# Kernel tuning notes

Measured on AMD Instinct MI355X. Metric: run time of the kernel, lower is better.

## Reference

```python
import jax, jax.numpy as jnp
import numpy as np

N_ITER = 3  # affine-invariant Karcher mean iterations (mean_options['n_iterations'])
EPS = 1e-12


def _sym(A):
    return 0.5 * (A + jnp.swapaxes(A, -1, -2))


def _eig_fun(A, fn):
    # Apply spectral function fn to symmetric matrix/matrices A: V diag(fn(w)) V^T
    w, V = jnp.linalg.eigh(A)
    return jnp.einsum('...ij,...j,...kj->...ik', V, fn(w), V)


def _logm(A):
    return _eig_fun(A, lambda w: jnp.log(jnp.maximum(w, EPS)))


def _expm(A):
    return _eig_fun(A, jnp.exp)


def _sqrtm(A):
    return _eig_fun(A, lambda w: jnp.sqrt(jnp.maximum(w, 0.0)))


def _invsqrtm(A):
    return _eig_fun(A, lambda w: 1.0 / jnp.sqrt(jnp.maximum(w, EPS)))


def _affine_invariant_mean(data, n_iterations):
    # Karcher mean: init at arithmetic mean, fixed-point iterations on the manifold
    M = jnp.mean(data, axis=0)
    for _ in range(n_iterations):
        Ms = _sqrtm(M)
        Mi = _invsqrtm(M)
        T = jnp.mean(_logm(Mi @ data @ Mi), axis=0)  # (n, n) tangent mean
        M = Ms @ _expm(T) @ Ms
    return _sym(M)


def setup_inputs() -> dict:
    key = jax.random.key(0)
    k1, k2 = jax.random.split(key)
    B, n = 8192, 64
    X = jax.random.normal(k1, (B, n, n), dtype=jnp.float32)
    # SPD batch: X X^T / n + 0.1 I
    data = jnp.einsum('bij,bkj->bik', X, X) / n + 0.1 * jnp.eye(n, dtype=jnp.float32)
    bias_param = 0.1 * jax.random.normal(k2, (n, n), dtype=jnp.float32)
    return {"data": data, "bias_param": bias_param}


def reference(data, bias_param):
    # 1) batch mean on the SPD manifold (affine-invariant Karcher mean)
    mean = _affine_invariant_mean(data, N_ITER)
    # 2) whitening: G data G with G = mean^{-1/2}
    G = _invsqrtm(mean)
    data_normalized = G @ data @ G
    # 3) bias congruence: Covbias = expm(sym(bias_param)) (log-Euclidean param),
    #    S = Covbias^{1/2} = expm(sym(bias_param)/2); out = S X S
    S = _eig_fun(_sym(bias_param), lambda w: jnp.exp(0.5 * w))
    return S @ data_normalized @ S
```

## Files before the change

### kernel.cpp

```cpp
#include <hip/hip_runtime.h>
#include <cmath>

#ifndef M_PI
#define M_PI 3.14159265358979323846
#endif

#define K_CHEB 48
#define A_CHEB 0.05
#define B_CHEB 14.0
#define PS_S 7
#define PS_Q 6

typedef __attribute__((ext_vector_type(8))) short bhalf8;
typedef __attribute__((ext_vector_type(16))) float f32x16;

struct PSArg {
  float mid, invhalf;
  float a[PS_Q + 1][PS_S];
};


__device__ __forceinline__ unsigned cvt_pk_bf16(float a, float b) {
  unsigned r;
  asm("v_cvt_pk_bf16_f32 %0, %1, %2" : "=v"(r) : "v"(a), "v"(b));
  return r;
}

__device__ __forceinline__ void split4_store(short* __restrict__ Xh, short* __restrict__ Xl,
                                             int off, float v0, float v1, float v2, float v3) {
  unsigned h01 = cvt_pk_bf16(v0, v1);
  unsigned h23 = cvt_pk_bf16(v2, v3);
  float r0 = v0 - __uint_as_float(h01 << 16);
  float r1 = v1 - __uint_as_float(h01 & 0xffff0000u);
  float r2 = v2 - __uint_as_float(h23 << 16);
  float r3 = v3 - __uint_as_float(h23 & 0xffff0000u);
  unsigned l01 = cvt_pk_bf16(r0, r1);
  unsigned l23 = cvt_pk_bf16(r2, r3);
  *(uint2*)(Xh + off) = make_uint2(h01, h23);
  *(uint2*)(Xl + off) = make_uint2(l01, l23);
}


__device__ __forceinline__ void stage64(const float* __restrict__ g, float* __restrict__ s, int tid) {
#pragma unroll
  for (int r = 0; r < 4; r++) {
    int idx = tid + 256 * r;
    *(float4*)(s + 4 * idx) = *(const float4*)(g + 4 * idx);
  }
}

__device__ __forceinline__ void store_tile(float* __restrict__ S, int r0, int c0, const float t[16]) {
#pragma unroll
  for (int i = 0; i < 4; i++)
    *(float4*)(S + (r0 + i) * 64 + c0) = *(const float4*)(&t[4 * i]);
}

__device__ __forceinline__ void gemm_tile_sym(const float* __restrict__ A, const float* __restrict__ B,
                                              int r0, int c0, float t[16]) {
#pragma unroll
  for (int i = 0; i < 16; i++) t[i] = 0.f;
#pragma unroll 4
  for (int k = 0; k < 64; k += 4) {
    float a[16], b[16];
#pragma unroll
    for (int kk = 0; kk < 4; kk++) {
      *(float4*)(&a[4 * kk]) = *(const float4*)(A + (k + kk) * 64 + r0);
      *(float4*)(&b[4 * kk]) = *(const float4*)(B + (k + kk) * 64 + c0);
    }
#pragma unroll
    for (int kk = 0; kk < 4; kk++)
#pragma unroll
      for (int i = 0; i < 4; i++)
#pragma unroll
        for (int j = 0; j < 4; j++)
          t[4 * i + j] += a[4 * kk + i] * b[4 * kk + j];
  }
}


__global__ __launch_bounds__(256) void reduce_mean8(const float* __restrict__ data,
                                                    float* __restrict__ part) {
  const size_t base = (size_t)blockIdx.x * 8 * 4096;
  const int tid = threadIdx.x;
#pragma unroll
  for (int r = 0; r < 4; r++) {
    int idx = tid + 256 * r;
    float4 s = make_float4(0.f, 0.f, 0.f, 0.f);
#pragma unroll
    for (int m = 0; m < 8; m++) {
      float4 v = *(const float4*)(data + base + (size_t)m * 4096 + 4 * idx);
      s.x += v.x; s.y += v.y; s.z += v.z; s.w += v.w;
    }
    *(float4*)(part + (size_t)blockIdx.x * 4096 + 4 * idx) = s;
  }
}

__global__ __launch_bounds__(256) void reduce_cols(const float* __restrict__ part,
                                                   float* __restrict__ outv,
                                                   int nparts, float scale) {
  __shared__ float s[3][64];
  const int jj = threadIdx.x & 63, gg = threadIdx.x >> 6;
  const int j = (blockIdx.x << 6) + jj;
  float sum = 0.f;
  for (int g = gg; g < nparts; g += 4)
    sum += part[(size_t)g * 4096 + j];
  if (gg) s[gg - 1][jj] = sum;
  __syncthreads();
  if (gg == 0) outv[j] = (sum + s[0][jj] + s[1][jj] + s[2][jj]) * scale;
}


#define LDX 72
#define MAT (64 * LDX)

__device__ __forceinline__ void load_afrags(const short* __restrict__ Xh, const short* __restrict__ Xl,
                                            int aoff, bhalf8 ah[4], bhalf8 al[4]) {
#pragma unroll
  for (int kb = 0; kb < 4; kb++) {
    ah[kb] = *(const bhalf8*)(Xh + aoff + 16 * kb);
    al[kb] = *(const bhalf8*)(Xl + aoff + 16 * kb);
  }
}

__device__ __forceinline__ f32x16 prod3(const bhalf8 ah[4], const bhalf8 al[4],
                                        const short* __restrict__ Bh, const short* __restrict__ Bl,
                                        int boff) {
  f32x16 acc;
#pragma unroll
  for (int t = 0; t < 16; t++) acc[t] = 0.f;
#pragma unroll
  for (int kb = 0; kb < 4; kb++) {
    bhalf8 bh = *(const bhalf8*)(Bh + boff + 16 * kb);
    bhalf8 bl = *(const bhalf8*)(Bl + boff + 16 * kb);
    acc = __builtin_amdgcn_mfma_f32_32x32x16_bf16(ah[kb], bh, acc, 0, 0, 0);
    acc = __builtin_amdgcn_mfma_f32_32x32x16_bf16(ah[kb], bl, acc, 0, 0, 0);
    acc = __builtin_amdgcn_mfma_f32_32x32x16_bf16(al[kb], bh, acc, 0, 0, 0);
  }
  return acc;
}

__device__ __forceinline__ void tstore16(short* __restrict__ Xh, short* __restrict__ Xl,
                                         int bcol, int R, int half, const f32x16 v) {
#pragma unroll
  for (int g = 0; g < 4; g++) {
    int off = bcol * LDX + 32 * R + 8 * g + 4 * half;
    split4_store(Xh, Xl, off, v[4 * g + 0], v[4 * g + 1], v[4 * g + 2], v[4 * g + 3]);
  }
}

__device__ __forceinline__ void stage_split(const float* __restrict__ g64,
                                            short* __restrict__ Xh, short* __restrict__ Xl,
                                            int tid) {
#pragma unroll
  for (int i = 0; i < 4; i++) {
    int idx = tid + 256 * i;
    float4 v = *(const float4*)(g64 + 4 * idx);
    int row = idx >> 4, col = (idx & 15) << 2;
    split4_store(Xh, Xl, row * LDX + col, v.x, v.y, v.z, v.w);
  }
}

__global__ __launch_bounds__(256, 2) void cheb_ps(const float* __restrict__ data,
                                                  const float* __restrict__ Mi,
                                                  float* __restrict__ partial,
                                                  PSArg co) {
  extern __shared__ __align__(16) short smem[];
  short* sMh  = smem;
  short* sMl  = sMh + MAT;
  short* sAh  = sMl + MAT;
  short* sAl  = sAh + MAT;
  short* sB0h = sAl + MAT;
  short* sB0l = sB0h + MAT;
  short* sB1h = sB0l + MAT;
  short* sB1l = sB1h + MAT;

  const int tid = threadIdx.x;
  const int lane = tid & 63, wv = tid >> 6;
  const int R = wv >> 1, C = wv & 1;
  const int ln31 = lane & 31, half = lane >> 5;
  const int aoff = (32 * R + ln31) * LDX + half * 8;
  const int bcol = 32 * C + ln31;
  const int boff = bcol * LDX + half * 8;
  const int dsel = bcol - 32 * R - 4 * half;

  stage_split(Mi, sMh, sMl, tid);

  f32x16 accTm;
#pragma unroll
  for (int t = 0; t < 16; t++) accTm[t] = 0.f;

  bhalf8 ah[4], al[4];
  __syncthreads();

#pragma unroll 1
  for (int m = 0; m < 8; m++) {
    stage_split(data + ((size_t)blockIdx.x * 8 + m) * 4096, sAh, sAl, tid);
    __syncthreads();

    load_afrags(sAh, sAl, aoff, ah, al);
    f32x16 acc = prod3(ah, al, sMh, sMl, boff);
    tstore16(sB0h, sB0l, bcol, R, half, acc);
    __syncthreads();

    load_afrags(sMh, sMl, aoff, ah, al);
    acc = prod3(ah, al, sB0h, sB0l, boff);
    f32x16 T1;
#pragma unroll
    for (int g = 0; g < 4; g++)
#pragma unroll
      for (int t = 0; t < 4; t++) {
        float a = acc[4 * g + t];
        if (8 * g + t == dsel) a -= co.mid;
        T1[4 * g + t] = a * co.invhalf;
      }
    tstore16(sAh, sAl, bcol, R, half, T1);
    __syncthreads();

    load_afrags(sAh, sAl, aoff, ah, al);

    f32x16 T2, T3, T4, T5, T6;
    acc = prod3(ah, al, sAh, sAl, boff);
#pragma unroll
    for (int g = 0; g < 4; g++)
#pragma unroll
      for (int t = 0; t < 4; t++)
        T2[4 * g + t] = 2.f * acc[4 * g + t] - ((8 * g + t == dsel) ? 1.f : 0.f);
    tstore16(sB0h, sB0l, bcol, R, half, T2);
    __syncthreads();

    acc = prod3(ah, al, sB0h, sB0l, boff);
#pragma unroll
    for (int t = 0; t < 16; t++) T3[t] = 2.f * acc[t] - T1[t];
    tstore16(sB1h, sB1l, bcol, R, half, T3);
    __syncthreads();

    acc = prod3(ah, al, sB1h, sB1l, boff);
#pragma unroll
    for (int t = 0; t < 16; t++) T4[t] = 2.f * acc[t] - T2[t];
    tstore16(sB0h, sB0l, bcol, R, half, T4);
    __syncthreads();

    acc = prod3(ah, al, sB0h, sB0l, boff);
#pragma unroll
    for (int t = 0; t < 16; t++) T5[t] = 2.f * acc[t] - T3[t];
    tstore16(sB1h, sB1l, bcol, R, half, T5);
    __syncthreads();

    acc = prod3(ah, al, sB1h, sB1l, boff);
#pragma unroll
    for (int t = 0; t < 16; t++) T6[t] = 2.f * acc[t] - T4[t];
    tstore16(sB1h == sB1h ? sB0h : sB0h, sB0l, bcol, R, half, T6);
    __syncthreads();

    acc = prod3(ah, al, sB0h, sB0l, boff);
    f32x16 Y7;
#pragma unroll
    for (int t = 0; t < 16; t++) Y7[t] = 2.f * acc[t] - T5[t];
    tstore16(sAh, sAl, bcol, R, half, Y7);
    __syncthreads();

    load_afrags(sAh, sAl, aoff, ah, al);
    f32x16 bq1, bq2;
#pragma unroll
    for (int g = 0; g < 4; g++)
#pragma unroll
      for (int t = 0; t < 4; t++) {
        int i = 4 * g + t;
        float v = co.a[6][1] * T1[i] + co.a[6][2] * T2[i] + co.a[6][3] * T3[i]
                + co.a[6][4] * T4[i] + co.a[6][5] * T5[i] + co.a[6][6] * T6[i];
        if (8 * g + t == dsel) v += co.a[6][0];
        bq1[i] = v; bq2[i] = 0.f;
      }
    tstore16(sB1h, sB1l, bcol, R, half, bq1);
    __syncthreads();

#pragma unroll
    for (int q = 5; q >= 1; q--) {
      const short* rh = (q & 1) ? sB1h : sB0h;
      const short* rl = (q & 1) ? sB1l : sB0l;
      short* wh = (q & 1) ? sB0h : sB1h;
      short* wl = (q & 1) ? sB0l : sB1l;
      acc = prod3(ah, al, rh, rl, boff);
      f32x16 nb;
#pragma unroll
      for (int g = 0; g < 4; g++)
#pragma unroll
        for (int t = 0; t < 4; t++) {
          int i = 4 * g + t;
          float gq = co.a[q][1] * T1[i] + co.a[q][2] * T2[i] + co.a[q][3] * T3[i]
                   + co.a[q][4] * T4[i] + co.a[q][5] * T5[i] + co.a[q][6] * T6[i];
          if (8 * g + t == dsel) gq += co.a[q][0];
          nb[i] = gq + 2.f * acc[i] - bq2[i];
        }
      bq2 = bq1; bq1 = nb;
      tstore16(wh, wl, bcol, R, half, bq1);
      __syncthreads();
    }

    acc = prod3(ah, al, sB0h, sB0l, boff);
#pragma unroll
    for (int g = 0; g < 4; g++)
#pragma unroll
      for (int t = 0; t < 4; t++) {
        int i = 4 * g + t;
        float g0 = co.a[0][1] * T1[i] + co.a[0][2] * T2[i] + co.a[0][3] * T3[i]
                 + co.a[0][4] * T4[i] + co.a[0][5] * T5[i] + co.a[0][6] * T6[i];
        if (8 * g + t == dsel) g0 += co.a[0][0];
        accTm[i] += g0 + acc[i] - bq2[i];
      }
  }

  float* pp = partial + (size_t)blockIdx.x * 4096;
#pragma unroll
  for (int g = 0; g < 4; g++)
#pragma unroll
    for (int t = 0; t < 4; t++)
      pp[(32 * R + 8 * g + 4 * half + t) * 64 + bcol] = accTm[4 * g + t];
}


__global__ __launch_bounds__(256) void invsqrt_series(const float* __restrict__ Min,
                                                      float* __restrict__ MiOut,
                                                      float* __restrict__ MsOut) {
  __shared__ float sM[4096], sE[4096], sE2[4096], sE3[4096];
  __shared__ float csh;
  const int tid = threadIdx.x;
  const int r0 = (tid >> 4) << 2, c0 = (tid & 15) << 2;

  stage64(Min, sM, tid);
  __syncthreads();
  if (tid == 0) {
    float s = 0.f;
    for (int i = 0; i < 64; i++) s += sM[i * 64 + i];
    csh = s * (1.f / 64.f);
  }
  __syncthreads();
  const float invc = 1.f / csh;
  for (int idx = tid; idx < 4096; idx += 256) {
    int r = idx >> 6, c = idx & 63;
    sE[idx] = 0.5f * (sM[idx] + sM[c * 64 + r]) * invc - ((r == c) ? 1.f : 0.f);
  }
  __syncthreads();

  float t[16];
  gemm_tile_sym(sE, sE, r0, c0, t);  store_tile(sE2, r0, c0, t); __syncthreads();
  gemm_tile_sym(sE2, sE, r0, c0, t); store_tile(sE3, r0, c0, t); __syncthreads();
  gemm_tile_sym(sE2, sE2, r0, c0, t); store_tile(sM, r0, c0, t); __syncthreads();
  float t5[16];
  gemm_tile_sym(sE2, sE3, r0, c0, t5);

  const float sc = sqrtf(csh), rsc = 1.f / sc;
#pragma unroll
  for (int i = 0; i < 4; i++)
#pragma unroll
    for (int j = 0; j < 4; j++) {
      int off = (r0 + i) * 64 + (c0 + j);
      float d = ((r0 + i) == (c0 + j)) ? 1.f : 0.f;
      float e = sE[off], e2 = sE2[off], e3 = sE3[off], e4 = sM[off], e5 = t5[4 * i + j];
      float mi = (d - 0.5f * e + 0.375f * e2 - 0.3125f * e3 + 0.2734375f * e4 - 0.24609375f * e5) * rsc;
      float ms = (d + 0.5f * e - 0.125f * e2 + 0.0625f * e3 - 0.0390625f * e4 + 0.02734375f * e5) * sc;
      MiOut[off] = mi;
      MsOut[off] = ms;
    }
}


__device__ void taylor_expm8(const float* __restrict__ sA, float* __restrict__ sR,
                             int tid, int r0, int c0, float postscale) {
  for (int idx = tid; idx < 4096; idx += 256) {
    int r = idx >> 6, c = idx & 63;
    sR[idx] = ((r == c) ? 1.f : 0.f) + sA[idx] * 0.125f;
  }
  __syncthreads();
  float t[16];
#pragma unroll 1
  for (int k = 7; k >= 1; k--) {
    gemm_tile_sym(sA, sR, r0, c0, t);
    __syncthreads();
    const float inv = 1.f / (float)k;
    const float fin = (k == 1) ? postscale : 1.f;
#pragma unroll
    for (int i = 0; i < 4; i++)
#pragma unroll
      for (int j = 0; j < 4; j++) {
        int off = (r0 + i) * 64 + (c0 + j);
        float d = ((r0 + i) == (c0 + j)) ? 1.f : 0.f;
        sR[off] = (d + t[4 * i + j] * inv) * fin;
      }
    __syncthreads();
  }
}

__global__ __launch_bounds__(256) void expm_update(const float* __restrict__ Tin,
                                                   const float* __restrict__ Msin,
                                                   float* __restrict__ Mout) {
  __shared__ float sA[4096], sR[4096], sB[4096];
  __shared__ float mush;
  const int tid = threadIdx.x;
  const int r0 = (tid >> 4) << 2, c0 = (tid & 15) << 2;

  stage64(Tin, sB, tid);
  __syncthreads();
  if (tid == 0) {
    float s = 0.f;
    for (int i = 0; i < 64; i++) s += sB[i * 64 + i];
    mush = s * (1.f / 64.f);
  }
  __syncthreads();
  const float mu = mush;
  for (int idx = tid; idx < 4096; idx += 256) {
    int r = idx >> 6, c = idx & 63;
    sA[idx] = 0.5f * (sB[idx] + sB[c * 64 + r]) - ((r == c) ? mu : 0.f);
  }
  __syncthreads();
  taylor_expm8(sA, sR, tid, r0, c0, expf(mu));

  stage64(Msin, sB, tid);
  __syncthreads();
  float t[16];
  gemm_tile_sym(sR, sB, r0, c0, t);
  store_tile(sA, r0, c0, t);
  __syncthreads();
  gemm_tile_sym(sB, sA, r0, c0, t);
#pragma unroll
  for (int i = 0; i < 4; i++)
    *(float4*)(Mout + (r0 + i) * 64 + c0) = *(const float4*)(&t[4 * i]);
}

__global__ __launch_bounds__(256) void bias_expm_P(const float* __restrict__ bias,
                                                   const float* __restrict__ Gin,
                                                   float* __restrict__ Pout) {
  __shared__ float sA[4096], sR[4096], sB[4096];
  const int tid = threadIdx.x;
  const int r0 = (tid >> 4) << 2, c0 = (tid & 15) << 2;

  stage64(bias, sB, tid);
  __syncthreads();
  for (int idx = tid; idx < 4096; idx += 256) {
    int r = idx >> 6, c = idx & 63;
    sA[idx] = 0.0625f * (sB[idx] + sB[c * 64 + r]);
  }
  __syncthreads();
  taylor_expm8(sA, sR, tid, r0, c0, 1.f);

  float t[16];
  gemm_tile_sym(sR, sR, r0, c0, t);
  store_tile(sB, r0, c0, t);
  __syncthreads();
  gemm_tile_sym(sB, sB, r0, c0, t);
  store_tile(sR, r0, c0, t);
  stage64(Gin, sA, tid);
  __syncthreads();
  gemm_tile_sym(sR, sA, r0, c0, t);
#pragma unroll
  for (int i = 0; i < 4; i++)
    *(float4*)(Pout + (r0 + i) * 64 + c0) = *(const float4*)(&t[4 * i]);
}

__global__ __launch_bounds__(256) void final_out(const float* __restrict__ data,
                                                 const float* __restrict__ Pin,
                                                 float* __restrict__ out) {
  __shared__ float sPT[4096], sD[4096], sT[4096];
  const int tid = threadIdx.x;
  const int r0 = (tid >> 4) << 2, c0 = (tid & 15) << 2;

  for (int idx = tid; idx < 4096; idx += 256) {
    int r = idx >> 6, c = idx & 63;
    sPT[c * 64 + r] = Pin[idx];
  }
  __syncthreads();
  float t[16];
#pragma unroll 1
  for (int m = 0; m < 8; m++) {
    size_t b = (size_t)blockIdx.x * 8 + m;
    stage64(data + b * 4096, sD, tid);
    __syncthreads();
    gemm_tile_sym(sD, sPT, r0, c0, t);
    store_tile(sT, r0, c0, t);
    __syncthreads();
    gemm_tile_sym(sPT, sT, r0, c0, t);
    float* ob = out + b * 4096;
#pragma unroll
    for (int i = 0; i < 4; i++)
      *(float4*)(ob + (r0 + i) * 64 + c0) = *(const float4*)(&t[4 * i]);
    __syncthreads();
  }
}


extern "C" void kernel_launch(void* const* d_in, const int* in_sizes, int n_in,
                              void* d_out, int out_size, void* d_ws, size_t ws_size,
                              hipStream_t stream) {
  const float* data = (const float*)d_in[0];
  const float* bias = (const float*)d_in[1];
  float* out = (float*)d_out;

  float* part = out;
  float* M  = (float*)d_ws;
  float* Mi = M + 4096;
  float* Ms = Mi + 4096;
  float* Tm = Ms + 4096;
  float* G  = Tm + 4096;
  float* P  = G + 4096;

  static bool attr_done = false;
  if (!attr_done) {
    hipFuncSetAttribute(reinterpret_cast<const void*>(cheb_ps),
                        hipFuncAttributeMaxDynamicSharedMemorySize,
                        8 * MAT * (int)sizeof(short));
    attr_done = true;
  }
  const int lds_bytes = 8 * MAT * (int)sizeof(short);

  PSArg co;
  {
    const double a = A_CHEB, b = B_CHEB;
    const int N = 256;
    double c[64] = {0};
    for (int j = 0; j <= K_CHEB; j++) {
      double s = 0.0;
      for (int k = 0; k < N; k++) {
        double th = M_PI * (k + 0.5) / N;
        double x = 0.5 * (a + b) + 0.5 * (b - a) * std::cos(th);
        s += std::log(x) * std::cos(j * th);
      }
      c[j] = 2.0 * s / N;
    }
    c[0] *= 0.5;
    double aa[PS_Q + 1][PS_S] = {};
    for (int q = PS_Q; q >= 1; --q) {
      for (int r = PS_S - 1; r >= 1; --r) {
        int k = q * PS_S + r;
        double av = 2.0 * c[k];
        aa[q][r] = av;
        c[k] -= av * 0.5;
        c[q * PS_S - r] -= av * 0.5;
      }
      aa[q][0] = c[q * PS_S];
      c[q * PS_S] = 0.0;
    }
    for (int r = 0; r < PS_S; r++) aa[0][r] = c[r];
    co.mid = (float)(0.5 * (a + b));
    co.invhalf = (float)(2.0 / (b - a));
    for (int q = 0; q <= PS_Q; q++)
      for (int r = 0; r < PS_S; r++) co.a[q][r] = (float)aa[q][r];
  }

  reduce_mean8<<<1024, 256, 0, stream>>>(data, part);
  reduce_cols<<<64, 256, 0, stream>>>(part, M, 1024, 1.f / 8192.f);

  for (int it = 0; it < 3; ++it) {
    invsqrt_series<<<1, 256, 0, stream>>>(M, Mi, Ms);
    cheb_ps<<<1024, 256, lds_bytes, stream>>>(data, Mi, part, co);
    reduce_cols<<<64, 256, 0, stream>>>(part, Tm, 1024, 1.f / 8192.f);
    expm_update<<<1, 256, 0, stream>>>(Tm, Ms, M);
  }

  invsqrt_series<<<1, 256, 0, stream>>>(M, G, Ms);
  bias_expm_P<<<1, 256, 0, stream>>>(bias, G, P);
  final_out<<<1024, 256, 0, stream>>>(data, P, out);
}
```

Measured before the change: 1.385 ms.

## Swizzle LDS layout, cut buffers for 3 blocks/CU, fuse expm with invsqrt

Replaces the padded LDS layout (stride 72) with an XOR-swizzled 64-wide layout and reduces the shared-memory buffers in cheb_ps from eight to six matrices. This frees enough LDS to target three blocks per CU, and the grid doubles to 2048 blocks with four matrices each. It also fuses expm_update with the following invsqrt_series into one single-block kernel, which removes launches from the serial chain. Trace reductions now use a wavefront shuffle instead of a single-thread loop. The risks are new bank-conflict patterns, an extra sync per matrix, and register pressure under the tighter launch bound.

```diff
diff --git a/kernel.cpp b/kernel.cpp
--- a/kernel.cpp
+++ b/kernel.cpp
@@ -77,6 +77,14 @@
   }
 }
 
+__device__ __forceinline__ float trace_bcast(const float* __restrict__ s) {
+  const int l = threadIdx.x & 63;
+  float d = s[l * 65];
+#pragma unroll
+  for (int o = 32; o > 0; o >>= 1) d += __shfl_down(d, o, 64);
+  return __shfl(d, 0, 64) * (1.f / 64.f);
+}
+
 
 __global__ __launch_bounds__(256) void reduce_mean8(const float* __restrict__ data,
                                                     float* __restrict__ part) {
@@ -110,28 +118,28 @@
 }
 
 
-#define LDX 72
-#define MAT (64 * LDX)
+#define SWZ(row, col) (((row) << 6) + ((col) ^ (((row) & 7) << 3)))
+#define MAT 4096
 
 __device__ __forceinline__ void load_afrags(const short* __restrict__ Xh, const short* __restrict__ Xl,
-                                            int aoff, bhalf8 ah[4], bhalf8 al[4]) {
+                                            const int ao[4], bhalf8 ah[4], bhalf8 al[4]) {
 #pragma unroll
   for (int kb = 0; kb < 4; kb++) {
-    ah[kb] = *(const bhalf8*)(Xh + aoff + 16 * kb);
-    al[kb] = *(const bhalf8*)(Xl + aoff + 16 * kb);
+    ah[kb] = *(const bhalf8*)(Xh + ao[kb]);
+    al[kb] = *(const bhalf8*)(Xl + ao[kb]);
   }
 }
 
 __device__ __forceinline__ f32x16 prod3(const bhalf8 ah[4], const bhalf8 al[4],
                                         const short* __restrict__ Bh, const short* __restrict__ Bl,
-                                        int boff) {
+                                        const int bo[4]) {
   f32x16 acc;
 #pragma unroll
   for (int t = 0; t < 16; t++) acc[t] = 0.f;
 #pragma unroll
   for (int kb = 0; kb < 4; kb++) {
-    bhalf8 bh = *(const bhalf8*)(Bh + boff + 16 * kb);
-    bhalf8 bl = *(const bhalf8*)(Bl + boff + 16 * kb);
+    bhalf8 bh = *(const bhalf8*)(Bh + bo[kb]);
+    bhalf8 bl = *(const bhalf8*)(Bl + bo[kb]);
     acc = __builtin_amdgcn_mfma_f32_32x32x16_bf16(ah[kb], bh, acc, 0, 0, 0);
     acc = __builtin_amdgcn_mfma_f32_32x32x16_bf16(ah[kb], bl, acc, 0, 0, 0);
     acc = __builtin_amdgcn_mfma_f32_32x32x16_bf16(al[kb], bh, acc, 0, 0, 0);
@@ -140,10 +148,11 @@
 }
 
 __device__ __forceinline__ void tstore16(short* __restrict__ Xh, short* __restrict__ Xl,
-                                         int bcol, int R, int half, const f32x16 v) {
+                                         int sbase, int xb, int R, int half, const f32x16 v) {
 #pragma unroll
   for (int g = 0; g < 4; g++) {
-    int off = bcol * LDX + 32 * R + 8 * g + 4 * half;
+    int m = 32 * R + 8 * g + 4 * half;
+    int off = sbase + (m ^ xb);
     split4_store(Xh, Xl, off, v[4 * g + 0], v[4 * g + 1], v[4 * g + 2], v[4 * g + 3]);
   }
 }
@@ -156,31 +165,42 @@
     int idx = tid + 256 * i;
     float4 v = *(const float4*)(g64 + 4 * idx);
     int row = idx >> 4, col = (idx & 15) << 2;
-    split4_store(Xh, Xl, row * LDX + col, v.x, v.y, v.z, v.w);
-  }
-}
-
-__global__ __launch_bounds__(256, 2) void cheb_ps(const float* __restrict__ data,
+    split4_store(Xh, Xl, SWZ(row, col), v.x, v.y, v.z, v.w);
+  }
+}
+
+__global__ __launch_bounds__(256, 3) void cheb_ps(const float* __restrict__ data,
                                                   const float* __restrict__ Mi,
                                                   float* __restrict__ partial,
                                                   PSArg co) {
   extern __shared__ __align__(16) short smem[];
-  short* sMh  = smem;
-  short* sMl  = sMh + MAT;
-  short* sAh  = sMl + MAT;
-  short* sAl  = sAh + MAT;
-  short* sB0h = sAl + MAT;
-  short* sB0l = sB0h + MAT;
-  short* sB1h = sB0l + MAT;
-  short* sB1l = sB1h + MAT;
+  short* sMh = smem;
+  short* sMl = sMh + MAT;
+  short* sAh = sMl + MAT;
+  short* sAl = sAh + MAT;
+  short* sBh = sAl + MAT;
+  short* sBl = sBh + MAT;
 
   const int tid = threadIdx.x;
   const int lane = tid & 63, wv = tid >> 6;
   const int R = wv >> 1, C = wv & 1;
   const int ln31 = lane & 31, half = lane >> 5;
-  const int aoff = (32 * R + ln31) * LDX + half * 8;
+  const int arow = 32 * R + ln31;
   const int bcol = 32 * C + ln31;
-  const int boff = bcol * LDX + half * 8;
+  int ao[4], bo[4];
+  {
+    const int abase = (arow << 6) + ((half * 8) ^ ((arow & 1) << 3));
+    const int a13 = (arow >> 1) & 3;
+    const int bbase = (bcol << 6) + ((half * 8) ^ ((bcol & 1) << 3));
+    const int b13 = (bcol >> 1) & 3;
+#pragma unroll
+    for (int kb = 0; kb < 4; kb++) {
+      ao[kb] = abase + 16 * (kb ^ a13);
+      bo[kb] = bbase + 16 * (kb ^ b13);
+    }
+  }
+  const int sbase = bcol << 6;
+  const int xb = (bcol & 7) << 3;
   const int dsel = bcol - 32 * R - 4 * half;
 
   stage_split(Mi, sMh, sMl, tid);
@@ -193,17 +213,17 @@
   __syncthreads();
 
 #pragma unroll 1
-  for (int m = 0; m < 8; m++) {
-    stage_split(data + ((size_t)blockIdx.x * 8 + m) * 4096, sAh, sAl, tid);
-    __syncthreads();
-
-    load_afrags(sAh, sAl, aoff, ah, al);
-    f32x16 acc = prod3(ah, al, sMh, sMl, boff);
-    tstore16(sB0h, sB0l, bcol, R, half, acc);
-    __syncthreads();
-
-    load_afrags(sMh, sMl, aoff, ah, al);
-    acc = prod3(ah, al, sB0h, sB0l, boff);
+  for (int m = 0; m < 4; m++) {
+    stage_split(data + ((size_t)blockIdx.x * 4 + m) * 4096, sAh, sAl, tid);
+    __syncthreads();
+
+    load_afrags(sAh, sAl, ao, ah, al);
+    f32x16 acc = prod3(ah, al, sMh, sMl, bo);
+    tstore16(sBh, sBl, sbase, xb, R, half, acc);
+    __syncthreads();
+
+    load_afrags(sMh, sMl, ao, ah, al);
+    acc = prod3(ah, al, sBh, sBl, bo);
     f32x16 T1;
 #pragma unroll
     for (int g = 0; g < 4; g++)
@@ -213,53 +233,53 @@
         if (8 * g + t == dsel) a -= co.mid;
         T1[4 * g + t] = a * co.invhalf;
       }
-    tstore16(sAh, sAl, bcol, R, half, T1);
-    __syncthreads();
-
-    load_afrags(sAh, sAl, aoff, ah, al);
+    tstore16(sAh, sAl, sbase, xb, R, half, T1);
+    __syncthreads();
+
+    load_afrags(sAh, sAl, ao, ah, al);
 
     f32x16 T2, T3, T4, T5, T6;
-    acc = prod3(ah, al, sAh, sAl, boff);
+    acc = prod3(ah, al, sAh, sAl, bo);
 #pragma unroll
     for (int g = 0; g < 4; g++)
 #pragma unroll
       for (int t = 0; t < 4; t++)
         T2[4 * g + t] = 2.f * acc[4 * g + t] - ((8 * g + t == dsel) ? 1.f : 0.f);
-    tstore16(sB0h, sB0l, bcol, R, half, T2);
-    __syncthreads();
-
-    acc = prod3(ah, al, sB0h, sB0l, boff);
+    tstore16(sBh, sBl, sbase, xb, R, half, T2);
+    __syncthreads();
+
+    acc = prod3(ah, al, sBh, sBl, bo);
 #pragma unroll
     for (int t = 0; t < 16; t++) T3[t] = 2.f * acc[t] - T1[t];
-    tstore16(sB1h, sB1l, bcol, R, half, T3);
-    __syncthreads();
-
-    acc = prod3(ah, al, sB1h, sB1l, boff);
+    tstore16(sAh, sAl, sbase, xb, R, half, T3);
+    __syncthreads();
+
+    acc = prod3(ah, al, sAh, sAl, bo);
 #pragma unroll
     for (int t = 0; t < 16; t++) T4[t] = 2.f * acc[t] - T2[t];
-    tstore16(sB0h, sB0l, bcol, R, half, T4);
-    __syncthreads();
-
-    acc = prod3(ah, al, sB0h, sB0l, boff);
+    tstore16(sBh, sBl, sbase, xb, R, half, T4);
+    __syncthreads();
+
+    acc = prod3(ah, al, sBh, sBl, bo);
 #pragma unroll
     for (int t = 0; t < 16; t++) T5[t] = 2.f * acc[t] - T3[t];
-    tstore16(sB1h, sB1l, bcol, R, half, T5);
-    __syncthreads();
-
-    acc = prod3(ah, al, sB1h, sB1l, boff);
+    tstore16(sAh, sAl, sbase, xb, R, half, T5);
+    __syncthreads();
+
+    acc = prod3(ah, al, sAh, sAl, bo);
 #pragma unroll
     for (int t = 0; t < 16; t++) T6[t] = 2.f * acc[t] - T4[t];
-    tstore16(sB1h == sB1h ? sB0h : sB0h, sB0l, bcol, R, half, T6);
-    __syncthreads();
-
-    acc = prod3(ah, al, sB0h, sB0l, boff);
+    tstore16(sBh, sBl, sbase, xb, R, half, T6);
+    __syncthreads();
+
+    acc = prod3(ah, al, sBh, sBl, bo);
     f32x16 Y7;
 #pragma unroll
     for (int t = 0; t < 16; t++) Y7[t] = 2.f * acc[t] - T5[t];
-    tstore16(sAh, sAl, bcol, R, half, Y7);
-    __syncthreads();
-
-    load_afrags(sAh, sAl, aoff, ah, al);
+    tstore16(sAh, sAl, sbase, xb, R, half, Y7);
+    __syncthreads();
+
+    load_afrags(sAh, sAl, ao, ah, al);
     f32x16 bq1, bq2;
 #pragma unroll
     for (int g = 0; g < 4; g++)
@@ -271,16 +291,16 @@
         if (8 * g + t == dsel) v += co.a[6][0];
         bq1[i] = v; bq2[i] = 0.f;
       }
-    tstore16(sB1h, sB1l, bcol, R, half, bq1);
+    tstore16(sBh, sBl, sbase, xb, R, half, bq1);
     __syncthreads();
 
 #pragma unroll
     for (int q = 5; q >= 1; q--) {
-      const short* rh = (q & 1) ? sB1h : sB0h;
-      const short* rl = (q & 1) ? sB1l : sB0l;
-      short* wh = (q & 1) ? sB0h : sB1h;
-      short* wl = (q & 1) ? sB0l : sB1l;
-      acc = prod3(ah, al, rh, rl, boff);
+      const short* rh = (q & 1) ? sBh : sAh;
+      const short* rl = (q & 1) ? sBl : sAl;
+      short* wh = (q & 1) ? sAh : sBh;
+      short* wl = (q & 1) ? sAl : sBl;
+      acc = prod3(ah, al, rh, rl, bo);
       f32x16 nb;
 #pragma unroll
       for (int g = 0; g < 4; g++)
@@ -293,11 +313,11 @@
           nb[i] = gq + 2.f * acc[i] - bq2[i];
         }
       bq2 = bq1; bq1 = nb;
-      tstore16(wh, wl, bcol, R, half, bq1);
+      tstore16(wh, wl, sbase, xb, R, half, bq1);
       __syncthreads();
     }
 
-    acc = prod3(ah, al, sB0h, sB0l, boff);
+    acc = prod3(ah, al, sAh, sAl, bo);
 #pragma unroll
     for (int g = 0; g < 4; g++)
 #pragma unroll
@@ -308,6 +328,7 @@
         if (8 * g + t == dsel) g0 += co.a[0][0];
         accTm[i] += g0 + acc[i] - bq2[i];
       }
+    __syncthreads();
   }
 
   float* pp = partial + (size_t)blockIdx.x * 4096;
@@ -323,18 +344,12 @@
                                                       float* __restrict__ MiOut,
                                                       float* __restrict__ MsOut) {
   __shared__ float sM[4096], sE[4096], sE2[4096], sE3[4096];
-  __shared__ float csh;
   const int tid = threadIdx.x;
   const int r0 = (tid >> 4) << 2, c0 = (tid & 15) << 2;
 
   stage64(Min, sM, tid);
   __syncthreads();
-  if (tid == 0) {
-    float s = 0.f;
-    for (int i = 0; i < 64; i++) s += sM[i * 64 + i];
-    csh = s * (1.f / 64.f);
-  }
-  __syncthreads();
+  const float csh = trace_bcast(sM);
   const float invc = 1.f / csh;
   for (int idx = tid; idx < 4096; idx += 256) {
     int r = idx >> 6, c = idx & 63;
@@ -391,40 +406,61 @@
   }
 }
 
-__global__ __launch_bounds__(256) void expm_update(const float* __restrict__ Tin,
-                                                   const float* __restrict__ Msin,
-                                                   float* __restrict__ Mout) {
-  __shared__ float sA[4096], sR[4096], sB[4096];
-  __shared__ float mush;
+
+__global__ __launch_bounds__(256) void expm_invsqrt(const float* __restrict__ Tin,
+                                                    const float* __restrict__ Msin,
+                                                    float* __restrict__ MiOut,
+                                                    float* __restrict__ MsOut) {
+  __shared__ float s0[4096], s1[4096], s2[4096], s3[4096], s4[4096];
   const int tid = threadIdx.x;
   const int r0 = (tid >> 4) << 2, c0 = (tid & 15) << 2;
-
-  stage64(Tin, sB, tid);
-  __syncthreads();
-  if (tid == 0) {
-    float s = 0.f;
-    for (int i = 0; i < 64; i++) s += sB[i * 64 + i];
-    mush = s * (1.f / 64.f);
-  }
-  __syncthreads();
-  const float mu = mush;
+  float t[16];
+
+  stage64(Tin, s0, tid);
+  __syncthreads();
+  const float mu = trace_bcast(s0);
   for (int idx = tid; idx < 4096; idx += 256) {
     int r = idx >> 6, c = idx & 63;
-    sA[idx] = 0.5f * (sB[idx] + sB[c * 64 + r]) - ((r == c) ? mu : 0.f);
-  }
-  __syncthreads();
-  taylor_expm8(sA, sR, tid, r0, c0, expf(mu));
-
-  stage64(Msin, sB, tid);
-  __syncthreads();
-  float t[16];
-  gemm_tile_sym(sR, sB, r0, c0, t);
-  store_tile(sA, r0, c0, t);
-  __syncthreads();
-  gemm_tile_sym(sB, sA, r0, c0, t);
+    s1[idx] = 0.5f * (s0[idx] + s0[c * 64 + r]) - ((r == c) ? mu : 0.f);
+  }
+  __syncthreads();
+  taylor_expm8(s1, s2, tid, r0, c0, expf(mu));
+
+  stage64(Msin, s0, tid);
+  __syncthreads();
+  gemm_tile_sym(s2, s0, r0, c0, t);
+  store_tile(s3, r0, c0, t);
+  __syncthreads();
+  gemm_tile_sym(s0, s3, r0, c0, t);
+  store_tile(s4, r0, c0, t);
+  __syncthreads();
+
+  const float csh = trace_bcast(s4);
+  const float invc = 1.f / csh;
+  for (int idx = tid; idx < 4096; idx += 256) {
+    int r = idx >> 6, c = idx & 63;
+    s0[idx] = 0.5f * (s4[idx] + s4[c * 64 + r]) * invc - ((r == c) ? 1.f : 0.f);
+  }
+  __syncthreads();
+  gemm_tile_sym(s0, s0, r0, c0, t);  store_tile(s1, r0, c0, t); __syncthreads();
+  gemm_tile_sym(s1, s0, r0, c0, t);  store_tile(s2, r0, c0, t); __syncthreads();
+  gemm_tile_sym(s1, s1, r0, c0, t);  store_tile(s3, r0, c0, t); __syncthreads();
+  float t5[16];
+  gemm_tile_sym(s1, s2, r0, c0, t5);
+
+  const float sc = sqrtf(csh), rsc = 1.f / sc;
 #pragma unroll
   for (int i = 0; i < 4; i++)
-    *(float4*)(Mout + (r0 + i) * 64 + c0) = *(const float4*)(&t[4 * i]);
+#pragma unroll
+    for (int j = 0; j < 4; j++) {
+      int off = (r0 + i) * 64 + (c0 + j);
+      float d = ((r0 + i) == (c0 + j)) ? 1.f : 0.f;
+      float e = s0[off], e2 = s1[off], e3 = s2[off], e4 = s3[off], e5 = t5[4 * i + j];
+      float mi = (d - 0.5f * e + 0.375f * e2 - 0.3125f * e3 + 0.2734375f * e4 - 0.24609375f * e5) * rsc;
+      float ms = (d + 0.5f * e - 0.125f * e2 + 0.0625f * e3 - 0.0390625f * e4 + 0.02734375f * e5) * sc;
+      MiOut[off] = mi;
+      MsOut[off] = ms;
+    }
 }
 
 __global__ __launch_bounds__(256) void bias_expm_P(const float* __restrict__ bias,
@@ -500,17 +536,9 @@
   float* Mi = M + 4096;
   float* Ms = Mi + 4096;
   float* Tm = Ms + 4096;
-  float* G  = Tm + 4096;
-  float* P  = G + 4096;
-
-  static bool attr_done = false;
-  if (!attr_done) {
-    hipFuncSetAttribute(reinterpret_cast<const void*>(cheb_ps),
-                        hipFuncAttributeMaxDynamicSharedMemorySize,
-                        8 * MAT * (int)sizeof(short));
-    attr_done = true;
-  }
-  const int lds_bytes = 8 * MAT * (int)sizeof(short);
+  float* P  = Tm + 4096;
+
+  const int lds_bytes = 6 * MAT * (int)sizeof(short);
 
   PSArg co;
   {
@@ -548,15 +576,14 @@
 
   reduce_mean8<<<1024, 256, 0, stream>>>(data, part);
   reduce_cols<<<64, 256, 0, stream>>>(part, M, 1024, 1.f / 8192.f);
+  invsqrt_series<<<1, 256, 0, stream>>>(M, Mi, Ms);
 
   for (int it = 0; it < 3; ++it) {
-    invsqrt_series<<<1, 256, 0, stream>>>(M, Mi, Ms);
-    cheb_ps<<<1024, 256, lds_bytes, stream>>>(data, Mi, part, co);
-    reduce_cols<<<64, 256, 0, stream>>>(part, Tm, 1024, 1.f / 8192.f);
-    expm_update<<<1, 256, 0, stream>>>(Tm, Ms, M);
-  }
-
-  invsqrt_series<<<1, 256, 0, stream>>>(M, G, Ms);
-  bias_expm_P<<<1, 256, 0, stream>>>(bias, G, P);
+    cheb_ps<<<2048, 256, lds_bytes, stream>>>(data, Mi, part, co);
+    reduce_cols<<<64, 256, 0, stream>>>(part, Tm, 2048, 1.f / 8192.f);
+    expm_invsqrt<<<1, 256, 0, stream>>>(Tm, Ms, Mi, Ms);
+  }
+
+  bias_expm_P<<<1, 256, 0, stream>>>(bias, Mi, P);
   final_out<<<1024, 256, 0, stream>>>(data, P, out);
 }
```

After: 3.402 ms. 146% more time.

## Fuse expm update with inverse-sqrt, add MFMA priority, vectorize Chebyshev updates

Applied to the files above, without the earlier changes.

Merges the single-block expm_update and invsqrt_series kernels into one expm_invsqrt kernel, which removes one tiny launch per Karcher iteration and the global round trip of M. The serial thread-0 trace loops are replaced with a wavefront shuffle reduction. It also raises wave priority around the MFMA sequences with s_setprio, and rewrites the per-element Chebyshev recurrences as vector operations using a precomputed diagonal mask. An extra __syncthreads is added at the end of each matrix loop iteration, and Ms is read and written in place by the same single block.

```diff
diff --git a/kernel.cpp b/kernel.cpp
--- a/kernel.cpp
+++ b/kernel.cpp
@@ -77,6 +77,14 @@
   }
 }
 
+__device__ __forceinline__ float trace_bcast(const float* __restrict__ s) {
+  const int l = threadIdx.x & 63;
+  float d = s[l * 65];
+#pragma unroll
+  for (int o = 32; o > 0; o >>= 1) d += __shfl_down(d, o, 64);
+  return __shfl(d, 0, 64) * (1.f / 64.f);
+}
+
 
 __global__ __launch_bounds__(256) void reduce_mean8(const float* __restrict__ data,
                                                     float* __restrict__ part) {
@@ -128,6 +136,7 @@
   f32x16 acc;
 #pragma unroll
   for (int t = 0; t < 16; t++) acc[t] = 0.f;
+  __builtin_amdgcn_s_setprio(1);
 #pragma unroll
   for (int kb = 0; kb < 4; kb++) {
     bhalf8 bh = *(const bhalf8*)(Bh + boff + 16 * kb);
@@ -136,6 +145,7 @@
     acc = __builtin_amdgcn_mfma_f32_32x32x16_bf16(ah[kb], bl, acc, 0, 0, 0);
     acc = __builtin_amdgcn_mfma_f32_32x32x16_bf16(al[kb], bh, acc, 0, 0, 0);
   }
+  __builtin_amdgcn_s_setprio(0);
   return acc;
 }
 
@@ -181,7 +191,13 @@
   const int aoff = (32 * R + ln31) * LDX + half * 8;
   const int bcol = 32 * C + ln31;
   const int boff = bcol * LDX + half * 8;
-  const int dsel = bcol - 32 * R - 4 * half;
+
+  f32x16 dg;
+#pragma unroll
+  for (int g = 0; g < 4; g++)
+#pragma unroll
+    for (int t = 0; t < 4; t++)
+      dg[4 * g + t] = ((32 * R + 8 * g + 4 * half + t) == bcol) ? 1.f : 0.f;
 
   stage_split(Mi, sMh, sMl, tid);
 
@@ -204,73 +220,48 @@
 
     load_afrags(sMh, sMl, aoff, ah, al);
     acc = prod3(ah, al, sB0h, sB0l, boff);
-    f32x16 T1;
-#pragma unroll
-    for (int g = 0; g < 4; g++)
-#pragma unroll
-      for (int t = 0; t < 4; t++) {
-        float a = acc[4 * g + t];
-        if (8 * g + t == dsel) a -= co.mid;
-        T1[4 * g + t] = a * co.invhalf;
-      }
+    f32x16 T1 = (acc - co.mid * dg) * co.invhalf;
     tstore16(sAh, sAl, bcol, R, half, T1);
     __syncthreads();
 
     load_afrags(sAh, sAl, aoff, ah, al);
 
-    f32x16 T2, T3, T4, T5, T6;
     acc = prod3(ah, al, sAh, sAl, boff);
-#pragma unroll
-    for (int g = 0; g < 4; g++)
-#pragma unroll
-      for (int t = 0; t < 4; t++)
-        T2[4 * g + t] = 2.f * acc[4 * g + t] - ((8 * g + t == dsel) ? 1.f : 0.f);
+    f32x16 T2 = 2.f * acc - dg;
     tstore16(sB0h, sB0l, bcol, R, half, T2);
     __syncthreads();
 
     acc = prod3(ah, al, sB0h, sB0l, boff);
-#pragma unroll
-    for (int t = 0; t < 16; t++) T3[t] = 2.f * acc[t] - T1[t];
+    f32x16 T3 = 2.f * acc - T1;
     tstore16(sB1h, sB1l, bcol, R, half, T3);
     __syncthreads();
 
     acc = prod3(ah, al, sB1h, sB1l, boff);
-#pragma unroll
-    for (int t = 0; t < 16; t++) T4[t] = 2.f * acc[t] - T2[t];
+    f32x16 T4 = 2.f * acc - T2;
     tstore16(sB0h, sB0l, bcol, R, half, T4);
     __syncthreads();
 
     acc = prod3(ah, al, sB0h, sB0l, boff);
-#pragma unroll
-    for (int t = 0; t < 16; t++) T5[t] = 2.f * acc[t] - T3[t];
+    f32x16 T5 = 2.f * acc - T3;
     tstore16(sB1h, sB1l, bcol, R, half, T5);
     __syncthreads();
 
     acc = prod3(ah, al, sB1h, sB1l, boff);
-#pragma unroll
-    for (int t = 0; t < 16; t++) T6[t] = 2.f * acc[t] - T4[t];
-    tstore16(sB1h == sB1h ? sB0h : sB0h, sB0l, bcol, R, half, T6);
+    f32x16 T6 = 2.f * acc - T4;
+    tstore16(sB0h, sB0l, bcol, R, half, T6);
     __syncthreads();
 
     acc = prod3(ah, al, sB0h, sB0l, boff);
-    f32x16 Y7;
-#pragma unroll
-    for (int t = 0; t < 16; t++) Y7[t] = 2.f * acc[t] - T5[t];
+    f32x16 Y7 = 2.f * acc - T5;
     tstore16(sAh, sAl, bcol, R, half, Y7);
     __syncthreads();
 
     load_afrags(sAh, sAl, aoff, ah, al);
-    f32x16 bq1, bq2;
-#pragma unroll
-    for (int g = 0; g < 4; g++)
-#pragma unroll
-      for (int t = 0; t < 4; t++) {
-        int i = 4 * g + t;
-        float v = co.a[6][1] * T1[i] + co.a[6][2] * T2[i] + co.a[6][3] * T3[i]
-                + co.a[6][4] * T4[i] + co.a[6][5] * T5[i] + co.a[6][6] * T6[i];
-        if (8 * g + t == dsel) v += co.a[6][0];
-        bq1[i] = v; bq2[i] = 0.f;
-      }
+    f32x16 bq1 = co.a[6][0] * dg + co.a[6][1] * T1 + co.a[6][2] * T2 + co.a[6][3] * T3
+               + co.a[6][4] * T4 + co.a[6][5] * T5 + co.a[6][6] * T6;
+    f32x16 bq2;
+#pragma unroll
+    for (int t = 0; t < 16; t++) bq2[t] = 0.f;
     tstore16(sB1h, sB1l, bcol, R, half, bq1);
     __syncthreads();
 
@@ -281,33 +272,19 @@
       short* wh = (q & 1) ? sB0h : sB1h;
       short* wl = (q & 1) ? sB0l : sB1l;
       acc = prod3(ah, al, rh, rl, boff);
-      f32x16 nb;
-#pragma unroll
-      for (int g = 0; g < 4; g++)
-#pragma unroll
-        for (int t = 0; t < 4; t++) {
-          int i = 4 * g + t;
-          float gq = co.a[q][1] * T1[i] + co.a[q][2] * T2[i] + co.a[q][3] * T3[i]
-                   + co.a[q][4] * T4[i] + co.a[q][5] * T5[i] + co.a[q][6] * T6[i];
-          if (8 * g + t == dsel) gq += co.a[q][0];
-          nb[i] = gq + 2.f * acc[i] - bq2[i];
-        }
+      f32x16 gq = co.a[q][0] * dg + co.a[q][1] * T1 + co.a[q][2] * T2 + co.a[q][3] * T3
+                + co.a[q][4] * T4 + co.a[q][5] * T5 + co.a[q][6] * T6;
+      f32x16 nb = gq + 2.f * acc - bq2;
       bq2 = bq1; bq1 = nb;
       tstore16(wh, wl, bcol, R, half, bq1);
       __syncthreads();
     }
 
     acc = prod3(ah, al, sB0h, sB0l, boff);
-#pragma unroll
-    for (int g = 0; g < 4; g++)
-#pragma unroll
-      for (int t = 0; t < 4; t++) {
-        int i = 4 * g + t;
-        float g0 = co.a[0][1] * T1[i] + co.a[0][2] * T2[i] + co.a[0][3] * T3[i]
-                 + co.a[0][4] * T4[i] + co.a[0][5] * T5[i] + co.a[0][6] * T6[i];
-        if (8 * g + t == dsel) g0 += co.a[0][0];
-        accTm[i] += g0 + acc[i] - bq2[i];
-      }
+    f32x16 g0 = co.a[0][0] * dg + co.a[0][1] * T1 + co.a[0][2] * T2 + co.a[0][3] * T3
+              + co.a[0][4] * T4 + co.a[0][5] * T5 + co.a[0][6] * T6;
+    accTm += g0 + acc - bq2;
+    __syncthreads();
   }
 
   float* pp = partial + (size_t)blockIdx.x * 4096;
@@ -323,18 +300,12 @@
                                                       float* __restrict__ MiOut,
                                                       float* __restrict__ MsOut) {
   __shared__ float sM[4096], sE[4096], sE2[4096], sE3[4096];
-  __shared__ float csh;
   const int tid = threadIdx.x;
   const int r0 = (tid >> 4) << 2, c0 = (tid & 15) << 2;
 
   stage64(Min, sM, tid);
   __syncthreads();
-  if (tid == 0) {
-    float s = 0.f;
-    for (int i = 0; i < 64; i++) s += sM[i * 64 + i];
-    csh = s * (1.f / 64.f);
-  }
-  __syncthreads();
+  const float csh = trace_bcast(sM);
   const float invc = 1.f / csh;
   for (int idx = tid; idx < 4096; idx += 256) {
     int r = idx >> 6, c = idx & 63;
@@ -391,40 +362,61 @@
   }
 }
 
-__global__ __launch_bounds__(256) void expm_update(const float* __restrict__ Tin,
-                                                   const float* __restrict__ Msin,
-                                                   float* __restrict__ Mout) {
-  __shared__ float sA[4096], sR[4096], sB[4096];
-  __shared__ float mush;
+
+__global__ __launch_bounds__(256) void expm_invsqrt(const float* __restrict__ Tin,
+                                                    const float* __restrict__ Msin,
+                                                    float* __restrict__ MiOut,
+                                                    float* __restrict__ MsOut) {
+  __shared__ float s0[4096], s1[4096], s2[4096], s3[4096], s4[4096];
   const int tid = threadIdx.x;
   const int r0 = (tid >> 4) << 2, c0 = (tid & 15) << 2;
-
-  stage64(Tin, sB, tid);
-  __syncthreads();
-  if (tid == 0) {
-    float s = 0.f;
-    for (int i = 0; i < 64; i++) s += sB[i * 64 + i];
-    mush = s * (1.f / 64.f);
-  }
-  __syncthreads();
-  const float mu = mush;
+  float t[16];
+
+  stage64(Tin, s0, tid);
+  __syncthreads();
+  const float mu = trace_bcast(s0);
   for (int idx = tid; idx < 4096; idx += 256) {
     int r = idx >> 6, c = idx & 63;
-    sA[idx] = 0.5f * (sB[idx] + sB[c * 64 + r]) - ((r == c) ? mu : 0.f);
-  }
-  __syncthreads();
-  taylor_expm8(sA, sR, tid, r0, c0, expf(mu));
-
-  stage64(Msin, sB, tid);
-  __syncthreads();
-  float t[16];
-  gemm_tile_sym(sR, sB, r0, c0, t);
-  store_tile(sA, r0, c0, t);
-  __syncthreads();
-  gemm_tile_sym(sB, sA, r0, c0, t);
+    s1[idx] = 0.5f * (s0[idx] + s0[c * 64 + r]) - ((r == c) ? mu : 0.f);
+  }
+  __syncthreads();
+  taylor_expm8(s1, s2, tid, r0, c0, expf(mu));
+
+  stage64(Msin, s0, tid);
+  __syncthreads();
+  gemm_tile_sym(s2, s0, r0, c0, t);
+  store_tile(s3, r0, c0, t);
+  __syncthreads();
+  gemm_tile_sym(s0, s3, r0, c0, t);
+  store_tile(s4, r0, c0, t);
+  __syncthreads();
+
+  const float csh = trace_bcast(s4);
+  const float invc = 1.f / csh;
+  for (int idx = tid; idx < 4096; idx += 256) {
+    int r = idx >> 6, c = idx & 63;
+    s0[idx] = 0.5f * (s4[idx] + s4[c * 64 + r]) * invc - ((r == c) ? 1.f : 0.f);
+  }
+  __syncthreads();
+  gemm_tile_sym(s0, s0, r0, c0, t);  store_tile(s1, r0, c0, t); __syncthreads();
+  gemm_tile_sym(s1, s0, r0, c0, t);  store_tile(s2, r0, c0, t); __syncthreads();
+  gemm_tile_sym(s1, s1, r0, c0, t);  store_tile(s3, r0, c0, t); __syncthreads();
+  float t5[16];
+  gemm_tile_sym(s1, s2, r0, c0, t5);
+
+  const float sc = sqrtf(csh), rsc = 1.f / sc;
 #pragma unroll
   for (int i = 0; i < 4; i++)
-    *(float4*)(Mout + (r0 + i) * 64 + c0) = *(const float4*)(&t[4 * i]);
+#pragma unroll
+    for (int j = 0; j < 4; j++) {
+      int off = (r0 + i) * 64 + (c0 + j);
+      float d = ((r0 + i) == (c0 + j)) ? 1.f : 0.f;
+      float e = s0[off], e2 = s1[off], e3 = s2[off], e4 = s3[off], e5 = t5[4 * i + j];
+      float mi = (d - 0.5f * e + 0.375f * e2 - 0.3125f * e3 + 0.2734375f * e4 - 0.24609375f * e5) * rsc;
+      float ms = (d + 0.5f * e - 0.125f * e2 + 0.0625f * e3 - 0.0390625f * e4 + 0.02734375f * e5) * sc;
+      MiOut[off] = mi;
+      MsOut[off] = ms;
+    }
 }
 
 __global__ __launch_bounds__(256) void bias_expm_P(const float* __restrict__ bias,
@@ -500,8 +492,7 @@
   float* Mi = M + 4096;
   float* Ms = Mi + 4096;
   float* Tm = Ms + 4096;
-  float* G  = Tm + 4096;
-  float* P  = G + 4096;
+  float* P  = Tm + 4096;
 
   static bool attr_done = false;
   if (!attr_done) {
@@ -548,15 +539,14 @@
 
   reduce_mean8<<<1024, 256, 0, stream>>>(data, part);
   reduce_cols<<<64, 256, 0, stream>>>(part, M, 1024, 1.f / 8192.f);
+  invsqrt_series<<<1, 256, 0, stream>>>(M, Mi, Ms);
 
   for (int it = 0; it < 3; ++it) {
-    invsqrt_series<<<1, 256, 0, stream>>>(M, Mi, Ms);
     cheb_ps<<<1024, 256, lds_bytes, stream>>>(data, Mi, part, co);
     reduce_cols<<<64, 256, 0, stream>>>(part, Tm, 1024, 1.f / 8192.f);
-    expm_update<<<1, 256, 0, stream>>>(Tm, Ms, M);
-  }
-
-  invsqrt_series<<<1, 256, 0, stream>>>(M, G, Ms);
-  bias_expm_P<<<1, 256, 0, stream>>>(bias, G, P);
+    expm_invsqrt<<<1, 256, 0, stream>>>(Tm, Ms, Mi, Ms);
+  }
+
+  bias_expm_P<<<1, 256, 0, stream>>>(bias, Mi, P);
   final_out<<<1024, 256, 0, stream>>>(data, P, out);
 }
```

Measured after the change: 1.777 ms. 28.3% more time.
